# Kernel tuning notes

Measured on AMD Instinct MI355X. Metric: run time of the kernel, lower is better.

The kernel has to match this reference:

```python
import jax, jax.numpy as jnp
import numpy as np

LAM = 1e-05
NUM_POINTS = 300
THRESHOLD = 0.5


def _sobel(img):
    # img: [B, 1, H, W] -> edge magnitude [B, 1, H, W]
    kx = jnp.array([[-1., 0., 1.], [-2., 0., 2.], [-1., 0., 1.]], jnp.float32).reshape(1, 1, 3, 3)
    ky = jnp.array([[-1., -2., -1.], [0., 0., 0.], [1., 2., 1.]], jnp.float32).reshape(1, 1, 3, 3)
    dn = jax.lax.conv_dimension_numbers(img.shape, kx.shape, ('NCHW', 'OIHW', 'NCHW'))
    ex = jax.lax.conv_general_dilated(img, kx, (1, 1), ((1, 1), (1, 1)), dimension_numbers=dn)
    ey = jax.lax.conv_general_dilated(img, ky, (1, 1), ((1, 1), (1, 1)), dimension_numbers=dn)
    return jnp.sqrt(ex ** 2 + ey ** 2)


def _select_points(edge_map, key):
    # JIT-friendly analogue of nonzero + randperm[:300]: random scores on
    # above-threshold pixels, take top NUM_POINTS; invalid slots are padded
    # with a duplicate of the first valid point (zero-length MST edges, so
    # they contribute nothing to total persistence, matching fewer points).
    H, W = edge_map.shape
    flat = edge_map.reshape(-1)
    mask = flat > THRESHOLD
    scores = jnp.where(mask, jax.random.uniform(key, flat.shape), -jnp.inf)
    _, idx = jax.lax.top_k(scores, NUM_POINTS)
    valid = mask[idx]
    pts = jnp.stack([idx // W, idx % W], axis=-1).astype(jnp.float32)  # (row, col)
    pts = jnp.where(valid[:, None], pts, pts[0])
    return pts


def _mst_total_persistence(pts):
    # H0 persistence of a Vietoris-Rips complex: births are 0, deaths are the
    # MST edge lengths (Prim's algorithm via lax.scan over N-1 steps).
    # total_persistence with exponent q=2: sum(death^2).
    d2 = jnp.sum((pts[:, None, :] - pts[None, :, :]) ** 2, axis=-1)
    D = jnp.sqrt(jnp.maximum(d2, 0.0))  # [N, N]
    n = pts.shape[0]
    in_tree = jnp.zeros((n,), dtype=bool).at[0].set(True)

    def step(carry, _):
        in_tree, mind = carry
        m = jnp.where(in_tree, jnp.inf, mind)
        j = jnp.argmin(m)
        w = m[j]
        in_tree = in_tree.at[j].set(True)
        mind = jnp.minimum(mind, D[j])
        return (in_tree, mind), w

    _, deaths = jax.lax.scan(step, (in_tree, D[0]), None, length=n - 1)
    return jnp.sum(deaths ** 2)


def _topo_loss(model_output, labels):
    pred_edges = _sobel(jax.nn.sigmoid(model_output))[:, 0]  # [B, H, W]
    mask_edges = _sobel(labels)[:, 0]                         # [B, H, W]
    B = pred_edges.shape[0]
    keys = jax.random.split(jax.random.key(42), 2 * B).reshape(B, 2)

    def per_sample(pe, me, k):
        pts_p = _select_points(pe, k[0])
        pts_m = _select_points(me, k[1])
        tp_p = _mst_total_persistence(pts_p)
        tp_m = _mst_total_persistence(pts_m)
        # SummaryStatisticLoss(total_persistence): |stat(mask) - stat(pred)|
        return jnp.abs(tp_m - tp_p)

    losses = jax.vmap(per_sample)(pred_edges, mask_edges, keys)
    return LAM * jnp.sum(losses) / B


def setup_inputs() -> dict:
    key = jax.random.key(0)
    k1, k2 = jax.random.split(key)
    model_output = jax.random.normal(k1, (32, 1, 512, 512), dtype=jnp.float32)
    labels = jax.random.uniform(k2, (32, 1, 512, 512), dtype=jnp.float32)
    return {"model_output": model_output, "labels": labels}


def reference(model_output, labels):
    return _topo_loss(model_output, labels)
```

## Files before the change

kernel.cpp:

```cpp
#include <hip/hip_runtime.h>
#include <cstdint>
#include <cstddef>

#define NPIX (512 * 512)
#define NMAPS 64
#define NPTS 300
#define CAP 2048
#define SLOTS 64
#define LBUFSZ 256
#define NWORDS 4096
#define TARGET 700.0
#define MT_BITS 0xFF63C000u

__device__ __forceinline__ uint32_t umin32(uint32_t a, uint32_t b) {
  return a < b ? a : b;
}

__device__ __forceinline__ void tf2x32(uint32_t k0, uint32_t k1,
                                       uint32_t x0, uint32_t x1,
                                       uint32_t& o0, uint32_t& o1) {
  uint32_t ks2 = k0 ^ k1 ^ 0x1BD11BDAu;
#define TFR(r) { x0 += x1; x1 = (x1 << (r)) | (x1 >> (32 - (r))); x1 ^= x0; }
  x0 += k0; x1 += k1;
  TFR(13) TFR(15) TFR(26) TFR(6)
  x0 += k1; x1 += ks2 + 1u;
  TFR(17) TFR(29) TFR(16) TFR(24)
  x0 += ks2; x1 += k0 + 2u;
  TFR(13) TFR(15) TFR(26) TFR(6)
  x0 += k0; x1 += k1 + 3u;
  TFR(17) TFR(29) TFR(16) TFR(24)
  x0 += k1; x1 += ks2 + 4u;
  TFR(13) TFR(15) TFR(26) TFR(6)
  x0 += ks2; x1 += k0 + 5u;
#undef TFR
  o0 = x0; o1 = x1;
}

__device__ __forceinline__ uint32_t score23(uint32_t k0, uint32_t k1, uint32_t p) {
  uint32_t a, b;
  tf2x32(k0, k1, 0u, p, a, b);
  return (a ^ b) >> 9;
}

__device__ __forceinline__ void map_key(int m, uint32_t& k0, uint32_t& k1) {
  tf2x32(0u, 42u, 0u, (uint32_t)m, k0, k1);
}

template <int CTRL>
__device__ __forceinline__ uint32_t dpp_mov_u32(uint32_t x) {
  return (uint32_t)__builtin_amdgcn_update_dpp((int)x, (int)x, CTRL, 0xF, 0xF,
                                               false);
}

template <int CTRL>
__device__ __forceinline__ uint32_t dpp_or0(uint32_t x) {
  return (uint32_t)__builtin_amdgcn_update_dpp(0, (int)x, CTRL, 0xF, 0xF,
                                               false);
}

__device__ __forceinline__ uint32_t wave_min_u32_bcast(uint32_t v) {
  v = umin32(v, dpp_mov_u32<0x111>(v));
  v = umin32(v, dpp_mov_u32<0x112>(v));
  v = umin32(v, dpp_mov_u32<0x114>(v));
  v = umin32(v, dpp_mov_u32<0x118>(v));
  v = umin32(v, dpp_mov_u32<0x142>(v));
  v = umin32(v, dpp_mov_u32<0x143>(v));
  return (uint32_t)__builtin_amdgcn_readlane((int)v, 63);
}

template <bool PRED, bool YIN>
__device__ __forceinline__ float4 ld4row(const float* __restrict__ src,
                                         int row, int X0) {
  if constexpr (!YIN) {
    if ((unsigned)row >= 512u) return make_float4(0.f, 0.f, 0.f, 0.f);
  }
  float4 v = *reinterpret_cast<const float4*>(src + (size_t)row * 512 + X0);
  if constexpr (PRED) {
    v.x = 1.f / (1.f + __expf(-v.x));
    v.y = 1.f / (1.f + __expf(-v.y));
    v.z = 1.f / (1.f + __expf(-v.z));
    v.w = 1.f / (1.f + __expf(-v.w));
  }
  return v;
}

template <bool PRED, bool YIN>
__device__ __forceinline__ float ldhrow(const float* __restrict__ src,
                                        int row, int hx, bool hact) {
  if (!hact) return 0.f;
  if constexpr (!YIN) {
    if ((unsigned)row >= 512u) return 0.f;
  }
  float t = src[(size_t)row * 512 + hx];
  if constexpr (PRED) t = 1.f / (1.f + __expf(-t));
  return t;
}

__device__ __forceinline__ void push_surv(unsigned long long* lbuf,
                                          unsigned int* lcnt, uint32_t x,
                                          uint32_t p) {
  unsigned int pos = atomicAdd(lcnt, 1u);
  if (pos < LBUFSZ)
    lbuf[pos] = ((unsigned long long)(x >> 9) << 32) | (uint32_t)(~p);
}

template <bool PRED, bool YIN>
__device__ __forceinline__ void edge_body(
    const float* __restrict__ src, unsigned long long* __restrict__ bitmap,
    unsigned int* __restrict__ wcnts, unsigned long long* lbuf,
    unsigned int* lcnt, int m, int l, int h, int r, int wi, uint32_t k0,
    uint32_t k1) {
  const int y0 = r * 8;
  const int X0 = h * 256 + l * 4;
  const int hx = 256 - h;
  const bool hact = h ? (l == 0) : (l == 63);
  const int lr = l & 15;

  float4 a = ld4row<PRED, YIN>(src, y0 - 1, X0);
  float4 b = ld4row<PRED, YIN>(src, y0, X0);
  float ha = ldhrow<PRED, YIN>(src, y0 - 1, hx, hact);
  float hb = ldhrow<PRED, YIN>(src, y0, hx, hact);
  float4 cn = ld4row<PRED, YIN>(src, y0 + 1, X0);
  float hcn = ldhrow<PRED, YIN>(src, y0 + 1, hx, hact);

  unsigned int cnt = 0;
  unsigned long long* __restrict__ bm =
      bitmap + (size_t)m * NWORDS + (h * 4 + (l >> 4));

#pragma unroll 2
  for (int i = 0; i < 8; ++i) {
    const int y = y0 + i;
    float4 c = cn;
    float hc = hcn;
    if (i < 7) {
      cn = ld4row<PRED, YIN>(src, y + 2, X0);
      hcn = ldhrow<PRED, YIN>(src, y + 2, hx, hact);
    }

    float t0 = a.x + 2.f * b.x + c.x, t1 = a.y + 2.f * b.y + c.y;
    float t2 = a.z + 2.f * b.z + c.z, t3 = a.w + 2.f * b.w + c.w;
    float u0 = c.x - a.x, u1 = c.y - a.y, u2 = c.z - a.z, u3 = c.w - a.w;
    float th = ha + 2.f * hb + hc, uh = hc - ha;

    float tU = __shfl_up(t3, 1), uU = __shfl_up(u3, 1);
    float tD = __shfl_down(t0, 1), uD = __shfl_down(u0, 1);
    if (l == 0) { tU = th; uU = uh; }
    if (l == 63) { tD = th; uD = uh; }

    float ex0 = t1 - tU, ex1 = t2 - t0, ex2 = t3 - t1, ex3 = tD - t2;
    float ey0 = uU + 2.f * u0 + u1, ey1 = u0 + 2.f * u1 + u2;
    float ey2 = u1 + 2.f * u2 + u3, ey3 = u2 + 2.f * u3 + uD;

    bool b0 = ex0 * ex0 + ey0 * ey0 > 0.25f;
    bool b1 = ex1 * ex1 + ey1 * ey1 > 0.25f;
    bool b2 = ex2 * ex2 + ey2 * ey2 > 0.25f;
    bool b3 = ex3 * ex3 + ey3 * ey3 > 0.25f;

    const uint32_t pb = (uint32_t)(y * 512 + X0);
    uint32_t q0, q1, q2, q3;
    { uint32_t o0, o1; tf2x32(k0, k1, 0u, pb + 0u, o0, o1); q0 = o0 ^ o1; }
    { uint32_t o0, o1; tf2x32(k0, k1, 0u, pb + 1u, o0, o1); q1 = o0 ^ o1; }
    { uint32_t o0, o1; tf2x32(k0, k1, 0u, pb + 2u, o0, o1); q2 = o0 ^ o1; }
    { uint32_t o0, o1; tf2x32(k0, k1, 0u, pb + 3u, o0, o1); q3 = o0 ^ o1; }

    if (b0 && q0 >= MT_BITS) push_surv(lbuf, lcnt, q0, pb + 0u);
    if (b1 && q1 >= MT_BITS) push_surv(lbuf, lcnt, q1, pb + 1u);
    if (b2 && q2 >= MT_BITS) push_surv(lbuf, lcnt, q2, pb + 2u);
    if (b3 && q3 >= MT_BITS) push_surv(lbuf, lcnt, q3, pb + 3u);

    uint32_t nib = (b0 ? 1u : 0u) | (b1 ? 2u : 0u) | (b2 ? 4u : 0u) |
                   (b3 ? 8u : 0u);
    unsigned long long full = (unsigned long long)nib << (4 * lr);
    uint32_t wlo = (uint32_t)full, whi = (uint32_t)(full >> 32);
    wlo |= dpp_or0<0x111>(wlo); whi |= dpp_or0<0x111>(whi);
    wlo |= dpp_or0<0x112>(wlo); whi |= dpp_or0<0x112>(whi);
    wlo |= dpp_or0<0x114>(wlo); whi |= dpp_or0<0x114>(whi);
    wlo |= dpp_or0<0x118>(wlo); whi |= dpp_or0<0x118>(whi);
    if (lr == 15) {
      unsigned long long word = ((unsigned long long)whi << 32) | wlo;
      bm[(size_t)y * 8] = word;
      cnt += (unsigned int)__popcll(word);
    }

    a = b; b = c; ha = hb; hb = hc;
  }

  cnt += __shfl_xor(cnt, 16);
  cnt += __shfl_xor(cnt, 32);
  if (l == 15) wcnts[m * 128 + wi] = cnt;
}

__global__ __launch_bounds__(256) void edge_collect_kernel(
    const float* __restrict__ mo, const float* __restrict__ lb,
    unsigned long long* __restrict__ bitmap, unsigned int* __restrict__ wcnts,
    unsigned long long* __restrict__ cand, unsigned int* __restrict__ bcnt,
    float* __restrict__ out) {
  const int m = blockIdx.y;
  const int which = m & 1;
  const int bx = blockIdx.x;
  const float* __restrict__ src = (which ? lb : mo) + (size_t)(m >> 1) * NPIX;
  const int l = threadIdx.x & 63;
  const int wi = bx * 4 + (threadIdx.x >> 6);
  const int h = wi & 1;
  const int r = wi >> 1;

  if (m == 0 && bx == 0 && threadIdx.x == 0) out[0] = 0.f;

  __shared__ unsigned long long lbuf[LBUFSZ];
  __shared__ unsigned int lcnt;
  if (threadIdx.x == 0) lcnt = 0;
  __syncthreads();

  uint32_t k0, k1;
  map_key(m, k0, k1);
  k0 = (uint32_t)__builtin_amdgcn_readfirstlane((int)k0);
  k1 = (uint32_t)__builtin_amdgcn_readfirstlane((int)k1);

  const bool yin = (r != 0) && (r != 63);
  if (which) {
    if (yin) edge_body<false, true>(src, bitmap, wcnts, lbuf, &lcnt, m, l, h, r, wi, k0, k1);
    else     edge_body<false, false>(src, bitmap, wcnts, lbuf, &lcnt, m, l, h, r, wi, k0, k1);
  } else {
    if (yin) edge_body<true, true>(src, bitmap, wcnts, lbuf, &lcnt, m, l, h, r, wi, k0, k1);
    else     edge_body<true, false>(src, bitmap, wcnts, lbuf, &lcnt, m, l, h, r, wi, k0, k1);
  }

  __syncthreads();
  const unsigned int total = lcnt;
  const unsigned int cc = total < SLOTS ? total : SLOTS;
  for (unsigned int i = threadIdx.x; i < cc; i += 256)
    cand[(size_t)m * CAP + bx * SLOTS + i] = lbuf[i];
  if (threadIdx.x == 0) bcnt[m * 32 + bx] = total;
}

__device__ __forceinline__ void reduce_N(const unsigned int* __restrict__ wcnts,
                                         int m, int tid, unsigned int* sN) {
  if (tid < 64) {
    unsigned int v = wcnts[m * 128 + tid] + wcnts[m * 128 + 64 + tid];
#pragma unroll
    for (int off = 32; off > 0; off >>= 1) v += __shfl_xor(v, off, 64);
    if (tid == 0) *sN = v;
  }
}

__global__ __launch_bounds__(256) void select_kernel(
    const unsigned long long* __restrict__ bitmap,
    const unsigned int* __restrict__ wcnts,
    const unsigned long long* __restrict__ cand,
    const unsigned int* __restrict__ bcnt,
    uint32_t* __restrict__ pts, unsigned int* __restrict__ nsel) {
  const int m = blockIdx.x;
  const int tid = threadIdx.x;
  __shared__ unsigned long long buf[CAP];
  __shared__ unsigned int hist[256];
  __shared__ unsigned int scnt32[32];
  __shared__ unsigned int sbase[33];
  __shared__ unsigned int s_tot, s_cnt, s_b, s_rank, sN, s_ovf;

  reduce_N(wcnts, m, tid, &sN);
  if (tid < 32) scnt32[tid] = bcnt[m * 32 + tid];
  __syncthreads();
  const unsigned int N = sN;
  if (N == 0) { if (tid == 0) nsel[m] = 0; return; }
  const unsigned int need = N < NPTS ? N : NPTS;

  if (tid == 0) {
    unsigned int s = 0, ovf = 0;
    for (int i = 0; i < 32; ++i) {
      sbase[i] = s;
      unsigned int cg = scnt32[i];
      if (cg > SLOTS) ovf = 1;
      s += cg < SLOTS ? cg : SLOTS;
    }
    sbase[32] = s;
    s_ovf = ovf;
  }
  __syncthreads();

  unsigned int c;
  if (!s_ovf && sbase[32] >= need) {
    c = sbase[32];
    const int g = tid >> 3, j0 = tid & 7;
    const unsigned int cg = scnt32[g] < SLOTS ? scnt32[g] : SLOTS;
    for (unsigned int i = j0; i < cg; i += 8)
      buf[sbase[g] + i] = cand[(size_t)m * CAP + g * SLOTS + i];
    __syncthreads();
  } else {
    uint32_t k0, k1;
    map_key(m, k0, k1);
    const unsigned long long* __restrict__ wmap = bitmap + (size_t)m * NWORDS;
    unsigned int mt = 0, cnt = 0;
    double target = TARGET;
    for (int iter = 0; iter < 16; ++iter) {
      mt = ((double)N > target)
               ? (unsigned int)(8388608.0 * (1.0 - target / (double)N))
               : 0u;
      if (tid == 0) s_tot = 0;
      __syncthreads();
      unsigned int lc = 0;
      for (int w = tid; w < NWORDS; w += 256) {
        unsigned long long word = wmap[w];
        while (word) {
          int bpos = __builtin_ctzll(word);
          word &= word - 1;
          uint32_t p = ((uint32_t)w << 6) + (uint32_t)bpos;
          lc += (score23(k0, k1, p) >= mt) ? 1u : 0u;
        }
      }
      if (lc) atomicAdd(&s_tot, lc);
      __syncthreads();
      cnt = s_tot;
      __syncthreads();
      if (cnt >= need && cnt <= CAP) break;
      if (cnt < need) target *= 3.0; else target *= 0.5;
    }
    if (tid == 0) s_cnt = 0;
    __syncthreads();
    for (int w = tid; w < NWORDS; w += 256) {
      unsigned long long word = wmap[w];
      while (word) {
        int bpos = __builtin_ctzll(word);
        word &= word - 1;
        uint32_t p = ((uint32_t)w << 6) + (uint32_t)bpos;
        uint32_t sc = score23(k0, k1, p);
        if (sc >= mt) {
          unsigned int pos = atomicAdd(&s_cnt, 1u);
          if (pos < CAP)
            buf[pos] = ((unsigned long long)sc << 32) | (uint32_t)(~p);
        }
      }
    }
    __syncthreads();
    c = s_cnt < CAP ? s_cnt : CAP;
    __syncthreads();
  }

  unsigned long long T = 0ull;
  if (c > need) {
    unsigned int rank = need;
    unsigned long long prefix = 0ull;
    for (int sh = 48; sh >= 0; sh -= 8) {
      hist[tid] = 0;
      __syncthreads();
      for (unsigned int i = tid; i < c; i += 256) {
        unsigned long long k = buf[i];
        if ((k >> (sh + 8)) == (prefix >> (sh + 8)))
          atomicAdd(&hist[(unsigned int)(k >> sh) & 255u], 1u);
      }
      __syncthreads();
      if (tid < 64) {
        unsigned int h0 = hist[4 * tid], h1 = hist[4 * tid + 1];
        unsigned int h2 = hist[4 * tid + 2], h3 = hist[4 * tid + 3];
        unsigned int gsum = h0 + h1 + h2 + h3;
        unsigned int s = gsum;
#pragma unroll
        for (int off = 1; off < 64; off <<= 1) {
          unsigned int o = __shfl_down(s, off, 64);
          s += (tid + off < 64) ? o : 0u;
        }
        unsigned int above = s - gsum;
        unsigned int S3 = above, S2 = S3 + h3, S1 = S2 + h2, S0 = S1 + h1;
        if (S3 < rank && rank <= S3 + h3) { s_b = 4 * tid + 3; s_rank = rank - S3; }
        if (S2 < rank && rank <= S2 + h2) { s_b = 4 * tid + 2; s_rank = rank - S2; }
        if (S1 < rank && rank <= S1 + h1) { s_b = 4 * tid + 1; s_rank = rank - S1; }
        if (S0 < rank && rank <= S0 + h0) { s_b = 4 * tid + 0; s_rank = rank - S0; }
      }
      __syncthreads();
      prefix |= ((unsigned long long)s_b) << sh;
      rank = s_rank;
    }
    T = prefix;
  }

  if (tid == 0) s_cnt = 0;
  __syncthreads();
  for (unsigned int i = tid; i < c; i += 256) {
    unsigned long long k = buf[i];
    if (k >= T) {
      unsigned int pos = atomicAdd(&s_cnt, 1u);
      if (pos < NPTS) {
        uint32_t p = ~(uint32_t)k;
        pts[(size_t)m * NPTS + pos] = ((p >> 9) << 16) | (p & 511u);
      }
    }
  }
  __syncthreads();
  if (tid == 0) nsel[m] = s_cnt < need ? s_cnt : need;
}

__global__ __launch_bounds__(128, 1) void mst_kernel(
    const uint32_t* __restrict__ pts, const unsigned int* __restrict__ nsel,
    float* __restrict__ out) {
  const int wv = threadIdx.x >> 6;
  const int m = blockIdx.x * 2 + wv;
  const int l = threadIdx.x & 63;
  const int n = (int)nsel[m];
  __shared__ float stp[2];

  unsigned int utp = 0;
  if (n > 1) {
    uint32_t pk[5], key[5];
    int px[5], py[5];
#pragma unroll
    for (int k = 0; k < 5; ++k) {
      int id = k * 64 + l;
      pk[k] = (id < n) ? pts[(size_t)m * NPTS + id] : 0u;
    }
    const uint32_t p0 = (uint32_t)__builtin_amdgcn_readlane((int)pk[0], 0);
    const int x0 = (int)(p0 >> 16), y0 = (int)(p0 & 0xFFFFu);
#pragma unroll
    for (int k = 0; k < 5; ++k) {
      int id = k * 64 + l;
      px[k] = (int)(pk[k] >> 16);
      py[k] = (int)(pk[k] & 0xFFFFu);
      if (id > 0 && id < n) {
        int dx = px[k] - x0, dy = py[k] - y0;
        key[k] = ((uint32_t)(__mul24(dx, dx) + __mul24(dy, dy)) << 9) |
                 (uint32_t)id;
      } else {
        key[k] = 0xFFFFFFFFu;
      }
    }

    for (int it = 0; it < n - 1; ++it) {
      uint32_t best = umin32(umin32(umin32(key[0], key[1]),
                                    umin32(key[2], key[3])), key[4]);
      best = wave_min_u32_bcast(best);
      utp += best >> 9;
      const int j = (int)(best & 511u);
      const int ko = j >> 6, lo = j & 63;
      uint32_t cp = pk[0];
#pragma unroll
      for (int k = 1; k < 5; ++k) cp = (ko == k) ? pk[k] : cp;
      const uint32_t pj = (uint32_t)__builtin_amdgcn_readlane((int)cp, lo);
      const int jx = (int)(pj >> 16), jy = (int)(pj & 0xFFFFu);
#pragma unroll
      for (int k = 0; k < 5; ++k) {
        int dx = px[k] - jx, dy = py[k] - jy;
        uint32_t nk = ((uint32_t)(__mul24(dx, dx) + __mul24(dy, dy)) << 9) |
                      (uint32_t)(k * 64 + l);
        uint32_t upd =
            (key[k] == 0xFFFFFFFFu) ? 0xFFFFFFFFu : umin32(key[k], nk);
        key[k] = (k == ko && l == lo) ? 0xFFFFFFFFu : upd;
      }
    }
  }
  if (l == 0) stp[wv] = (float)utp;
  __syncthreads();
  if (threadIdx.x == 0)
    atomicAdd(out, 1e-5f * fabsf(stp[1] - stp[0]) / 32.f);
}

extern "C" void kernel_launch(void* const* d_in, const int* in_sizes, int n_in,
                              void* d_out, int out_size, void* d_ws,
                              size_t ws_size, hipStream_t stream) {
  const float* mo = (const float*)d_in[0];
  const float* lb = (const float*)d_in[1];
  float* out = (float*)d_out;
  char* ws = (char*)d_ws;

  unsigned long long* bitmap = (unsigned long long*)ws;
  unsigned long long* cand = (unsigned long long*)(ws + 2097152);
  unsigned int* wcnts = (unsigned int*)(ws + 3145728);
  unsigned int* bcnt  = (unsigned int*)(ws + 3178496);
  unsigned int* nsel  = (unsigned int*)(ws + 3186688);
  uint32_t* pts       = (uint32_t*)(ws + 3186944);

  edge_collect_kernel<<<dim3(32, 64), 256, 0, stream>>>(mo, lb, bitmap, wcnts,
                                                        cand, bcnt, out);
  select_kernel<<<NMAPS, 256, 0, stream>>>(bitmap, wcnts, cand, bcnt, pts,
                                           nsel);
  mst_kernel<<<32, 128, 0, stream>>>(pts, nsel, out);
}
```

Baseline: 226.8 us.

## Process pred and mask maps together per block with 4-row strips and interleaved Threefry

Result: faster. 215.2 us (-5.1%).

```diff
diff --git a/kernel.cpp b/kernel.cpp
--- a/kernel.cpp
+++ b/kernel.cpp
@@ -6,21 +6,25 @@
 #define NMAPS 64
 #define NPTS 300
 #define CAP 2048
-#define SLOTS 64
-#define LBUFSZ 256
+#define SLOTS 32
+#define LBUFSZ 64
 #define NWORDS 4096
 #define TARGET 700.0
 #define MT_BITS 0xFF63C000u
 
 __device__ __forceinline__ uint32_t umin32(uint32_t a, uint32_t b) {
   return a < b ? a : b;
+}
+
+__device__ __forceinline__ uint32_t rotl32(uint32_t x, int r) {
+  return (x << r) | (x >> (32 - r));
 }
 
 __device__ __forceinline__ void tf2x32(uint32_t k0, uint32_t k1,
                                        uint32_t x0, uint32_t x1,
                                        uint32_t& o0, uint32_t& o1) {
   uint32_t ks2 = k0 ^ k1 ^ 0x1BD11BDAu;
-#define TFR(r) { x0 += x1; x1 = (x1 << (r)) | (x1 >> (32 - (r))); x1 ^= x0; }
+#define TFR(r) { x0 += x1; x1 = rotl32(x1, r); x1 ^= x0; }
   x0 += k0; x1 += k1;
   TFR(13) TFR(15) TFR(26) TFR(6)
   x0 += k1; x1 += ks2 + 1u;
@@ -36,6 +40,33 @@
   o0 = x0; o1 = x1;
 }
 
+__device__ __forceinline__ void tf4(uint32_t k0, uint32_t k1, uint32_t pb,
+                                    uint32_t& z0, uint32_t& z1, uint32_t& z2,
+                                    uint32_t& z3) {
+  const uint32_t ks2 = k0 ^ k1 ^ 0x1BD11BDAu;
+  const uint32_t s = pb + k1;
+  uint32_t a0 = k0, a1 = s;
+  uint32_t b0 = k0, b1 = s + 1u;
+  uint32_t c0 = k0, c1 = s + 2u;
+  uint32_t d0 = k0, d1 = s + 3u;
+#define R4(r)                                                         \
+  a0 += a1; b0 += b1; c0 += c1; d0 += d1;                             \
+  a1 = rotl32(a1, r); b1 = rotl32(b1, r);                             \
+  c1 = rotl32(c1, r); d1 = rotl32(d1, r);                             \
+  a1 ^= a0; b1 ^= b0; c1 ^= c0; d1 ^= d0;
+#define K4(ka, kb)                                                    \
+  a0 += (ka); b0 += (ka); c0 += (ka); d0 += (ka);                     \
+  a1 += (kb); b1 += (kb); c1 += (kb); d1 += (kb);
+  R4(13) R4(15) R4(26) R4(6)  K4(k1, ks2 + 1u)
+  R4(17) R4(29) R4(16) R4(24) K4(ks2, k0 + 2u)
+  R4(13) R4(15) R4(26) R4(6)  K4(k0, k1 + 3u)
+  R4(17) R4(29) R4(16) R4(24) K4(k1, ks2 + 4u)
+  R4(13) R4(15) R4(26) R4(6)  K4(ks2, k0 + 5u)
+#undef R4
+#undef K4
+  z0 = a0 ^ a1; z1 = b0 ^ b1; z2 = c0 ^ c1; z3 = d0 ^ d1;
+}
+
 __device__ __forceinline__ uint32_t score23(uint32_t k0, uint32_t k1, uint32_t p) {
   uint32_t a, b;
   tf2x32(k0, k1, 0u, p, a, b);
@@ -105,89 +136,87 @@
 }
 
 template <bool PRED, bool YIN>
-__device__ __forceinline__ void edge_body(
+__device__ __forceinline__ void part_body(
     const float* __restrict__ src, unsigned long long* __restrict__ bitmap,
     unsigned int* __restrict__ wcnts, unsigned long long* lbuf,
-    unsigned int* lcnt, int m, int l, int h, int r, int wi, uint32_t k0,
+    unsigned int* lcnt, int m, int l, int h, int qq, uint32_t k0,
     uint32_t k1) {
-  const int y0 = r * 8;
+  const int y0 = qq * 4;
   const int X0 = h * 256 + l * 4;
   const int hx = 256 - h;
   const bool hact = h ? (l == 0) : (l == 63);
   const int lr = l & 15;
 
-  float4 a = ld4row<PRED, YIN>(src, y0 - 1, X0);
-  float4 b = ld4row<PRED, YIN>(src, y0, X0);
-  float ha = ldhrow<PRED, YIN>(src, y0 - 1, hx, hact);
-  float hb = ldhrow<PRED, YIN>(src, y0, hx, hact);
-  float4 cn = ld4row<PRED, YIN>(src, y0 + 1, X0);
-  float hcn = ldhrow<PRED, YIN>(src, y0 + 1, hx, hact);
+  float4 fA = ld4row<PRED, YIN>(src, y0 - 1, X0);
+  float4 fB = ld4row<PRED, YIN>(src, y0 + 0, X0);
+  float4 fC = ld4row<PRED, YIN>(src, y0 + 1, X0);
+  float4 fD = ld4row<PRED, YIN>(src, y0 + 2, X0);
+  float sA = ldhrow<PRED, YIN>(src, y0 - 1, hx, hact);
+  float sB = ldhrow<PRED, YIN>(src, y0 + 0, hx, hact);
+  float sC = ldhrow<PRED, YIN>(src, y0 + 1, hx, hact);
+  float sD = ldhrow<PRED, YIN>(src, y0 + 2, hx, hact);
 
   unsigned int cnt = 0;
-  unsigned long long* __restrict__ bm =
-      bitmap + (size_t)m * NWORDS + (h * 4 + (l >> 4));
-
-#pragma unroll 2
-  for (int i = 0; i < 8; ++i) {
-    const int y = y0 + i;
-    float4 c = cn;
-    float hc = hcn;
-    if (i < 7) {
-      cn = ld4row<PRED, YIN>(src, y + 2, X0);
-      hcn = ldhrow<PRED, YIN>(src, y + 2, hx, hact);
-    }
-
-    float t0 = a.x + 2.f * b.x + c.x, t1 = a.y + 2.f * b.y + c.y;
-    float t2 = a.z + 2.f * b.z + c.z, t3 = a.w + 2.f * b.w + c.w;
-    float u0 = c.x - a.x, u1 = c.y - a.y, u2 = c.z - a.z, u3 = c.w - a.w;
-    float th = ha + 2.f * hb + hc, uh = hc - ha;
-
-    float tU = __shfl_up(t3, 1), uU = __shfl_up(u3, 1);
-    float tD = __shfl_down(t0, 1), uD = __shfl_down(u0, 1);
-    if (l == 0) { tU = th; uU = uh; }
-    if (l == 63) { tD = th; uD = uh; }
-
-    float ex0 = t1 - tU, ex1 = t2 - t0, ex2 = t3 - t1, ex3 = tD - t2;
-    float ey0 = uU + 2.f * u0 + u1, ey1 = u0 + 2.f * u1 + u2;
-    float ey2 = u1 + 2.f * u2 + u3, ey3 = u2 + 2.f * u3 + uD;
-
-    bool b0 = ex0 * ex0 + ey0 * ey0 > 0.25f;
-    bool b1 = ex1 * ex1 + ey1 * ey1 > 0.25f;
-    bool b2 = ex2 * ex2 + ey2 * ey2 > 0.25f;
-    bool b3 = ex3 * ex3 + ey3 * ey3 > 0.25f;
-
-    const uint32_t pb = (uint32_t)(y * 512 + X0);
-    uint32_t q0, q1, q2, q3;
-    { uint32_t o0, o1; tf2x32(k0, k1, 0u, pb + 0u, o0, o1); q0 = o0 ^ o1; }
-    { uint32_t o0, o1; tf2x32(k0, k1, 0u, pb + 1u, o0, o1); q1 = o0 ^ o1; }
-    { uint32_t o0, o1; tf2x32(k0, k1, 0u, pb + 2u, o0, o1); q2 = o0 ^ o1; }
-    { uint32_t o0, o1; tf2x32(k0, k1, 0u, pb + 3u, o0, o1); q3 = o0 ^ o1; }
-
-    if (b0 && q0 >= MT_BITS) push_surv(lbuf, lcnt, q0, pb + 0u);
-    if (b1 && q1 >= MT_BITS) push_surv(lbuf, lcnt, q1, pb + 1u);
-    if (b2 && q2 >= MT_BITS) push_surv(lbuf, lcnt, q2, pb + 2u);
-    if (b3 && q3 >= MT_BITS) push_surv(lbuf, lcnt, q3, pb + 3u);
-
-    uint32_t nib = (b0 ? 1u : 0u) | (b1 ? 2u : 0u) | (b2 ? 4u : 0u) |
-                   (b3 ? 8u : 0u);
-    unsigned long long full = (unsigned long long)nib << (4 * lr);
-    uint32_t wlo = (uint32_t)full, whi = (uint32_t)(full >> 32);
-    wlo |= dpp_or0<0x111>(wlo); whi |= dpp_or0<0x111>(whi);
-    wlo |= dpp_or0<0x112>(wlo); whi |= dpp_or0<0x112>(whi);
-    wlo |= dpp_or0<0x114>(wlo); whi |= dpp_or0<0x114>(whi);
-    wlo |= dpp_or0<0x118>(wlo); whi |= dpp_or0<0x118>(whi);
-    if (lr == 15) {
-      unsigned long long word = ((unsigned long long)whi << 32) | wlo;
-      bm[(size_t)y * 8] = word;
-      cnt += (unsigned int)__popcll(word);
-    }
-
-    a = b; b = c; ha = hb; hb = hc;
-  }
+  unsigned long long* __restrict__ bm2 =
+      bitmap + (size_t)m * NWORDS + (size_t)y0 * 8 + (h * 4 + (l >> 4));
+  uint32_t pbase = (uint32_t)(y0 * 512 + X0);
+
+#define ROWQ(RA, RB, RC, SA, SB, SC, II)                                      \
+  do {                                                                        \
+    float t0 = RA.x + 2.f * RB.x + RC.x, t1 = RA.y + 2.f * RB.y + RC.y;       \
+    float t2 = RA.z + 2.f * RB.z + RC.z, t3 = RA.w + 2.f * RB.w + RC.w;       \
+    float u0 = RC.x - RA.x, u1 = RC.y - RA.y;                                 \
+    float u2 = RC.z - RA.z, u3 = RC.w - RA.w;                                 \
+    float th = SA + 2.f * SB + SC, uh = SC - SA;                              \
+    float tU = __shfl_up(t3, 1), uU = __shfl_up(u3, 1);                       \
+    float tD = __shfl_down(t0, 1), uD = __shfl_down(u0, 1);                   \
+    if (l == 0) { tU = th; uU = uh; }                                         \
+    if (l == 63) { tD = th; uD = uh; }                                        \
+    float ex0 = t1 - tU, ex1 = t2 - t0, ex2 = t3 - t1, ex3 = tD - t2;         \
+    float ey0 = uU + 2.f * u0 + u1, ey1 = u0 + 2.f * u1 + u2;                 \
+    float ey2 = u1 + 2.f * u2 + u3, ey3 = u2 + 2.f * u3 + uD;                 \
+    uint32_t nib = (ex0 * ex0 + ey0 * ey0 > 0.25f ? 1u : 0u) |                \
+                   (ex1 * ex1 + ey1 * ey1 > 0.25f ? 2u : 0u) |                \
+                   (ex2 * ex2 + ey2 * ey2 > 0.25f ? 4u : 0u) |                \
+                   (ex3 * ex3 + ey3 * ey3 > 0.25f ? 8u : 0u);                 \
+    uint32_t z0, z1, z2, z3;                                                  \
+    tf4(k0, k1, pbase, z0, z1, z2, z3);                                       \
+    uint32_t qm = (z0 >= MT_BITS ? 1u : 0u) | (z1 >= MT_BITS ? 2u : 0u) |     \
+                  (z2 >= MT_BITS ? 4u : 0u) | (z3 >= MT_BITS ? 8u : 0u);      \
+    uint32_t sv = nib & qm;                                                   \
+    if (sv) {                                                                 \
+      if (sv & 1u) push_surv(lbuf, lcnt, z0, pbase);                          \
+      if (sv & 2u) push_surv(lbuf, lcnt, z1, pbase + 1u);                     \
+      if (sv & 4u) push_surv(lbuf, lcnt, z2, pbase + 2u);                     \
+      if (sv & 8u) push_surv(lbuf, lcnt, z3, pbase + 3u);                     \
+    }                                                                         \
+    unsigned long long full = (unsigned long long)nib << (4 * lr);            \
+    uint32_t wlo = (uint32_t)full, whi = (uint32_t)(full >> 32);              \
+    wlo |= dpp_or0<0x111>(wlo); whi |= dpp_or0<0x111>(whi);                   \
+    wlo |= dpp_or0<0x112>(wlo); whi |= dpp_or0<0x112>(whi);                   \
+    wlo |= dpp_or0<0x114>(wlo); whi |= dpp_or0<0x114>(whi);                   \
+    wlo |= dpp_or0<0x118>(wlo); whi |= dpp_or0<0x118>(whi);                   \
+    if (lr == 15) {                                                           \
+      unsigned long long word = ((unsigned long long)whi << 32) | wlo;        \
+      bm2[(II) * 8] = word;                                                   \
+      cnt += (unsigned int)__popcll(word);                                    \
+    }                                                                         \
+    pbase += 512u;                                                            \
+  } while (0)
+
+  ROWQ(fA, fB, fC, sA, sB, sC, 0);
+  fA = ld4row<PRED, YIN>(src, y0 + 3, X0);
+  sA = ldhrow<PRED, YIN>(src, y0 + 3, hx, hact);
+  ROWQ(fB, fC, fD, sB, sC, sD, 1);
+  fB = ld4row<PRED, YIN>(src, y0 + 4, X0);
+  sB = ldhrow<PRED, YIN>(src, y0 + 4, hx, hact);
+  ROWQ(fC, fD, fA, sC, sD, sA, 2);
+  ROWQ(fD, fA, fB, sD, sA, sB, 3);
+#undef ROWQ
 
   cnt += __shfl_xor(cnt, 16);
   cnt += __shfl_xor(cnt, 32);
-  if (l == 15) wcnts[m * 128 + wi] = cnt;
+  if (l == 15) wcnts[m * 256 + 2 * qq + h] = cnt;
 }
 
 __global__ __launch_bounds__(256) void edge_collect_kernel(
@@ -195,48 +224,61 @@
     unsigned long long* __restrict__ bitmap, unsigned int* __restrict__ wcnts,
     unsigned long long* __restrict__ cand, unsigned int* __restrict__ bcnt,
     float* __restrict__ out) {
-  const int m = blockIdx.y;
-  const int which = m & 1;
-  const int bx = blockIdx.x;
-  const float* __restrict__ src = (which ? lb : mo) + (size_t)(m >> 1) * NPIX;
+  const int b = blockIdx.x;
+  const int s = b >> 6;
+  const int j = b & 63;
+  const int v = threadIdx.x >> 6;
   const int l = threadIdx.x & 63;
-  const int wi = bx * 4 + (threadIdx.x >> 6);
-  const int h = wi & 1;
-  const int r = wi >> 1;
-
-  if (m == 0 && bx == 0 && threadIdx.x == 0) out[0] = 0.f;
-
-  __shared__ unsigned long long lbuf[LBUFSZ];
-  __shared__ unsigned int lcnt;
-  if (threadIdx.x == 0) lcnt = 0;
-  __syncthreads();
-
-  uint32_t k0, k1;
-  map_key(m, k0, k1);
-  k0 = (uint32_t)__builtin_amdgcn_readfirstlane((int)k0);
-  k1 = (uint32_t)__builtin_amdgcn_readfirstlane((int)k1);
-
-  const bool yin = (r != 0) && (r != 63);
-  if (which) {
-    if (yin) edge_body<false, true>(src, bitmap, wcnts, lbuf, &lcnt, m, l, h, r, wi, k0, k1);
-    else     edge_body<false, false>(src, bitmap, wcnts, lbuf, &lcnt, m, l, h, r, wi, k0, k1);
+  const int h = v & 1;
+  const int qq = 2 * j + (v >> 1);
+  const int mA = 2 * s;
+  const int mB = 2 * s + 1;
+  const float* __restrict__ srcP = mo + (size_t)s * NPIX;
+  const float* __restrict__ srcM = lb + (size_t)s * NPIX;
+
+  if (b == 0 && threadIdx.x == 0) out[0] = 0.f;
+
+  __shared__ unsigned long long lbufP[LBUFSZ], lbufM[LBUFSZ];
+  __shared__ unsigned int lcntP, lcntM;
+  if (threadIdx.x == 0) { lcntP = 0; lcntM = 0; }
+  __syncthreads();
+
+  uint32_t ka0, ka1, kb0, kb1;
+  map_key(mA, ka0, ka1);
+  map_key(mB, kb0, kb1);
+  ka0 = (uint32_t)__builtin_amdgcn_readfirstlane((int)ka0);
+  ka1 = (uint32_t)__builtin_amdgcn_readfirstlane((int)ka1);
+  kb0 = (uint32_t)__builtin_amdgcn_readfirstlane((int)kb0);
+  kb1 = (uint32_t)__builtin_amdgcn_readfirstlane((int)kb1);
+
+  const bool yin = (qq != 0) && (qq != 127);
+  if (yin) {
+    part_body<true, true>(srcP, bitmap, wcnts, lbufP, &lcntP, mA, l, h, qq, ka0, ka1);
+    part_body<false, true>(srcM, bitmap, wcnts, lbufM, &lcntM, mB, l, h, qq, kb0, kb1);
   } else {
-    if (yin) edge_body<true, true>(src, bitmap, wcnts, lbuf, &lcnt, m, l, h, r, wi, k0, k1);
-    else     edge_body<true, false>(src, bitmap, wcnts, lbuf, &lcnt, m, l, h, r, wi, k0, k1);
-  }
-
-  __syncthreads();
-  const unsigned int total = lcnt;
-  const unsigned int cc = total < SLOTS ? total : SLOTS;
-  for (unsigned int i = threadIdx.x; i < cc; i += 256)
-    cand[(size_t)m * CAP + bx * SLOTS + i] = lbuf[i];
-  if (threadIdx.x == 0) bcnt[m * 32 + bx] = total;
+    part_body<true, false>(srcP, bitmap, wcnts, lbufP, &lcntP, mA, l, h, qq, ka0, ka1);
+    part_body<false, false>(srcM, bitmap, wcnts, lbufM, &lcntM, mB, l, h, qq, kb0, kb1);
+  }
+
+  __syncthreads();
+  const unsigned int tP = lcntP, tM = lcntM;
+  const unsigned int ccP = tP < SLOTS ? tP : SLOTS;
+  const unsigned int ccM = tM < SLOTS ? tM : SLOTS;
+  for (unsigned int i = threadIdx.x; i < ccP; i += 256)
+    cand[(size_t)mA * CAP + j * SLOTS + i] = lbufP[i];
+  for (unsigned int i = threadIdx.x; i < ccM; i += 256)
+    cand[(size_t)mB * CAP + j * SLOTS + i] = lbufM[i];
+  if (threadIdx.x == 0) {
+    bcnt[mA * 64 + j] = tP;
+    bcnt[mB * 64 + j] = tM;
+  }
 }
 
 __device__ __forceinline__ void reduce_N(const unsigned int* __restrict__ wcnts,
                                          int m, int tid, unsigned int* sN) {
   if (tid < 64) {
-    unsigned int v = wcnts[m * 128 + tid] + wcnts[m * 128 + 64 + tid];
+    const unsigned int* w = wcnts + m * 256;
+    unsigned int v = w[tid] + w[tid + 64] + w[tid + 128] + w[tid + 192];
 #pragma unroll
     for (int off = 32; off > 0; off >>= 1) v += __shfl_xor(v, off, 64);
     if (tid == 0) *sN = v;
@@ -253,12 +295,12 @@
   const int tid = threadIdx.x;
   __shared__ unsigned long long buf[CAP];
   __shared__ unsigned int hist[256];
-  __shared__ unsigned int scnt32[32];
-  __shared__ unsigned int sbase[33];
+  __shared__ unsigned int scnt64[64];
+  __shared__ unsigned int sbase[65];
   __shared__ unsigned int s_tot, s_cnt, s_b, s_rank, sN, s_ovf;
 
   reduce_N(wcnts, m, tid, &sN);
-  if (tid < 32) scnt32[tid] = bcnt[m * 32 + tid];
+  if (tid < 64) scnt64[tid] = bcnt[m * 64 + tid];
   __syncthreads();
   const unsigned int N = sN;
   if (N == 0) { if (tid == 0) nsel[m] = 0; return; }
@@ -266,23 +308,23 @@
 
   if (tid == 0) {
     unsigned int s = 0, ovf = 0;
-    for (int i = 0; i < 32; ++i) {
+    for (int i = 0; i < 64; ++i) {
       sbase[i] = s;
-      unsigned int cg = scnt32[i];
+      unsigned int cg = scnt64[i];
       if (cg > SLOTS) ovf = 1;
       s += cg < SLOTS ? cg : SLOTS;
     }
-    sbase[32] = s;
+    sbase[64] = s;
     s_ovf = ovf;
   }
   __syncthreads();
 
   unsigned int c;
-  if (!s_ovf && sbase[32] >= need) {
-    c = sbase[32];
-    const int g = tid >> 3, j0 = tid & 7;
-    const unsigned int cg = scnt32[g] < SLOTS ? scnt32[g] : SLOTS;
-    for (unsigned int i = j0; i < cg; i += 8)
+  if (!s_ovf && sbase[64] >= need) {
+    c = sbase[64];
+    const int g = tid >> 2, j0 = tid & 3;
+    const unsigned int cg = scnt64[g] < SLOTS ? scnt64[g] : SLOTS;
+    for (unsigned int i = j0; i < cg; i += 4)
       buf[sbase[g] + i] = cand[(size_t)m * CAP + g * SLOTS + i];
     __syncthreads();
   } else {
@@ -462,12 +504,12 @@
   unsigned long long* bitmap = (unsigned long long*)ws;
   unsigned long long* cand = (unsigned long long*)(ws + 2097152);
   unsigned int* wcnts = (unsigned int*)(ws + 3145728);
-  unsigned int* bcnt  = (unsigned int*)(ws + 3178496);
-  unsigned int* nsel  = (unsigned int*)(ws + 3186688);
-  uint32_t* pts       = (uint32_t*)(ws + 3186944);
-
-  edge_collect_kernel<<<dim3(32, 64), 256, 0, stream>>>(mo, lb, bitmap, wcnts,
-                                                        cand, bcnt, out);
+  unsigned int* bcnt  = (unsigned int*)(ws + 3211264);
+  unsigned int* nsel  = (unsigned int*)(ws + 3227648);
+  uint32_t* pts       = (uint32_t*)(ws + 3227904);
+
+  edge_collect_kernel<<<2048, 256, 0, stream>>>(mo, lb, bitmap, wcnts,
+                                                cand, bcnt, out);
   select_kernel<<<NMAPS, 256, 0, stream>>>(bitmap, wcnts, cand, bcnt, pts,
                                            nsel);
   mst_kernel<<<32, 128, 0, stream>>>(pts, nsel, out);
```
